# Kernel tuning notes

Hardware: AMD Instinct MI355X
Metric: run time of the kernel (lower is better)

The kernel has to match this reference:

```python
import jax, jax.numpy as jnp
import numpy as np
from jax import lax

WEIGHT_PREC = 8
ACT_PREC = 8
ACT_BOUND = 6.0  # fixed symmetric activation bound (quant_act.bounds)
EPS = 1e-6


def _ste_round(v):
    # AQT round-to-nearest with straight-through estimator
    return v + lax.stop_gradient(jnp.floor(v + 0.5) - v)


def setup_inputs() -> dict:
    key = jax.random.key(0)
    k1, k2 = jax.random.split(key)
    B, D, F = 131072, 512, 512
    x = jax.random.normal(k1, (B, D), dtype=jnp.float32)
    # lecun_normal-style kernel init
    kernel = jax.random.normal(k2, (D, F), dtype=jnp.float32) * (1.0 / np.sqrt(D))
    bias = jnp.zeros((F,), dtype=jnp.float32)
    padding_mask = jnp.ones((B, 1), dtype=bool)
    return {"x": x, "kernel": kernel, "bias": bias, "padding_mask": padding_mask}


def reference(x, kernel, bias, padding_mask):
    # padding_mask only affects bounds statistics collection; with fixed act
    # bounds and train=False it does not enter the math.
    wmax = float(2 ** (WEIGHT_PREC - 1) - 1)  # 127
    amax = float(2 ** (ACT_PREC - 1) - 1)     # 127

    # per-channel weight quantization: axis=(0,), scale shape (1, features)
    w_bound = jnp.maximum(jnp.max(jnp.abs(kernel), axis=0, keepdims=True), EPS)
    w_scale = wmax / w_bound                   # (1, F)
    w_q = jnp.clip(_ste_round(kernel * w_scale), -wmax, wmax)

    # per-tensor symmetric activation quantization with fixed bound
    a_scale = amax / ACT_BOUND                 # scalar
    x_q = jnp.clip(_ste_round(x * a_scale), -amax, amax)

    # integer-valued dot_general, then dequantize by the combined scale
    y = jnp.einsum('bd,df->bf', x_q, w_q)      # [B, F]
    y = y / (a_scale * w_scale)                # broadcast (1, F)
    return y + bias[jnp.newaxis, :]
```

## Files before the change

### kernel.cpp

```cpp
#include <hip/hip_runtime.h>
#include <stdint.h>

typedef int   int32x4   __attribute__((ext_vector_type(4)));
typedef int   int32x16  __attribute__((ext_vector_type(16)));
typedef float floatx4   __attribute__((ext_vector_type(4)));

#define B_ROWS 131072
#define DK 512
#define FN 512
#define A_SCALE_F ((float)(127.0 / 6.0))

#define GBLK 256
#define GT   1024
#define BMS  32
#define GTILES (B_ROWS / BMS / GBLK)

__global__ void wq_quant_kernel(const float* __restrict__ kern,
                                int8_t* __restrict__ wq,
                                float* __restrict__ invcs) {
  __shared__ float smax[256];
  __shared__ float sscale[4];
  const int c = threadIdx.x & 3;
  const int g = threadIdx.x >> 2;
  const int col = blockIdx.x * 4 + c;

  float m = 0.f;
#pragma unroll
  for (int i = 0; i < 8; ++i) {
    m = fmaxf(m, fabsf(kern[(size_t)(g * 8 + i) * FN + col]));
  }
  smax[threadIdx.x] = m;
  __syncthreads();
  if (threadIdx.x < 4) {
    float mm = smax[threadIdx.x];
#pragma unroll 8
    for (int g2 = 1; g2 < 64; ++g2) mm = fmaxf(mm, smax[g2 * 4 + threadIdx.x]);
    const float wb = fmaxf(mm, 1e-6f);
    const float ws = 127.f / wb;
    sscale[threadIdx.x] = ws;
    invcs[blockIdx.x * 4 + threadIdx.x] =
        (float)(1.0 / ((double)A_SCALE_F * (double)ws));
  }
  __syncthreads();
  const float ws = sscale[c];
  uint32_t* wq32 = (uint32_t*)(wq + (size_t)col * DK);
#pragma unroll
  for (int d = 0; d < 2; ++d) {
    uint32_t p = 0;
#pragma unroll
    for (int j = 0; j < 4; ++j) {
      float v = kern[(size_t)(g * 8 + d * 4 + j) * FN + col] * ws;
      v = floorf(v + 0.5f);
      v = fminf(fmaxf(v, -127.f), 127.f);
      p |= ((uint32_t)((int)v & 255)) << (8 * j);
    }
    wq32[g * 2 + d] = p;
  }
}

__global__ __launch_bounds__(GT, 4)
void aqt_gemm_fused(const float* __restrict__ x,
                    const int8_t* __restrict__ wq,
                    const float* __restrict__ invcs,
                    const float* __restrict__ bias,
                    float* __restrict__ out) {
  __shared__ __align__(16) uint8_t xq[2][BMS * DK];

  const int tid  = threadIdx.x;
  const int lane = tid & 63;
  const int wv   = tid >> 6;
  const int l31  = lane & 31;
  const int l5   = lane >> 5;

  const int c4 = tid & 127;
  const int r0 = tid >> 7;

  const int col = wv * 32 + l31;
  int32x4 Bf[16];
#pragma unroll
  for (int ks = 0; ks < 16; ++ks)
    Bf[ks] = *(const int32x4*)(wq + (size_t)col * DK + ks * 32 + l5 * 16);
  const float inv = invcs[col];
  const float bv  = bias[col];

  const size_t row0 = (size_t)blockIdx.x * (GTILES * BMS);

  {
    const float* xg = x + row0 * DK;
    floatx4 v[4];
#pragma unroll
    for (int i = 0; i < 4; ++i)
      v[i] = *(const floatx4*)(xg + (size_t)(i * 8 + r0) * DK + c4 * 4);
#pragma unroll
    for (int i = 0; i < 4; ++i) {
      const int r = i * 8 + r0;
      uint32_t p = 0;
#pragma unroll
      for (int j = 0; j < 4; ++j) {
        float q = floorf(v[i][j] * A_SCALE_F + 0.5f);
        q = fminf(fmaxf(q, -127.f), 127.f);
        p |= ((uint32_t)((int)q & 255)) << (8 * j);
      }
      *(uint32_t*)(&xq[0][r * DK + ((c4 * 4) ^ ((r & 31) << 4))]) = p;
    }
  }
  asm volatile("s_waitcnt lgkmcnt(0)" ::: "memory");
  __builtin_amdgcn_s_barrier();

  for (int t = 0; t < GTILES; ++t) {
    const uint8_t* bufC = &xq[t & 1][0];
    uint8_t* bufN = &xq[(t & 1) ^ 1][0];
    const size_t rowT = row0 + (size_t)t * BMS;
    const bool pf = (t + 1 < GTILES);

    floatx4 v[4];
    if (pf) {
      const float* xg = x + (rowT + BMS) * DK;
#pragma unroll
      for (int i = 0; i < 4; ++i)
        v[i] = *(const floatx4*)(xg + (size_t)(i * 8 + r0) * DK + c4 * 4);
    }

    int32x16 acc = (int32x16)(0);
    const uint8_t* aRow = bufC + l31 * DK;
    const int aswz = l31 << 4;
#pragma unroll
    for (int ks = 0; ks < 16; ++ks) {
      int32x4 a = *(const int32x4*)(aRow + ((ks * 32 + l5 * 16) ^ aswz));
      acc = __builtin_amdgcn_mfma_i32_32x32x32_i8(a, Bf[ks], acc, 0, 0, 0);
    }

    if (pf) {
#pragma unroll
      for (int i = 0; i < 4; ++i) {
        const int r = i * 8 + r0;
        uint32_t p = 0;
#pragma unroll
        for (int j = 0; j < 4; ++j) {
          float q = floorf(v[i][j] * A_SCALE_F + 0.5f);
          q = fminf(fmaxf(q, -127.f), 127.f);
          p |= ((uint32_t)((int)q & 255)) << (8 * j);
        }
        *(uint32_t*)(&bufN[r * DK + ((c4 * 4) ^ ((r & 31) << 4))]) = p;
      }
    }

#pragma unroll
    for (int r = 0; r < 16; ++r) {
      const int rowl = (r & 3) + 8 * (r >> 2) + 4 * l5;
      out[(rowT + rowl) * FN + col] = (float)acc[r] * inv + bv;
    }

    asm volatile("s_waitcnt lgkmcnt(0)" ::: "memory");
    __builtin_amdgcn_s_barrier();
  }
}

extern "C" void kernel_launch(void* const* d_in, const int* in_sizes, int n_in,
                              void* d_out, int out_size, void* d_ws, size_t ws_size,
                              hipStream_t stream) {
  const float* x    = (const float*)d_in[0];
  const float* kern = (const float*)d_in[1];
  const float* bias = (const float*)d_in[2];

  int8_t* wq    = (int8_t*)d_ws;
  float*  invcs = (float*)((char*)d_ws + (size_t)FN * DK);

  wq_quant_kernel<<<128, 256, 0, stream>>>(kern, wq, invcs);
  aqt_gemm_fused<<<GBLK, GT, 0, stream>>>(x, wq, invcs, bias, (float*)d_out);
}
```

Baseline: 131.9 us.

## Deepen global-load prefetch to two tiles ahead with unrolled ping-pong loop

```diff
diff --git a/kernel.cpp b/kernel.cpp
--- a/kernel.cpp
+++ b/kernel.cpp
@@ -58,6 +58,17 @@
   }
 }
 
+__device__ __forceinline__ uint32_t quant4(floatx4 v) {
+  uint32_t p = 0;
+#pragma unroll
+  for (int j = 0; j < 4; ++j) {
+    float q = floorf(v[j] * A_SCALE_F + 0.5f);
+    q = fminf(fmaxf(q, -127.f), 127.f);
+    p |= ((uint32_t)((int)q & 255)) << (8 * j);
+  }
+  return p;
+}
+
 __global__ __launch_bounds__(GT, 4)
 void aqt_gemm_fused(const float* __restrict__ x,
                     const int8_t* __restrict__ wq,
@@ -85,75 +96,68 @@
 
   const size_t row0 = (size_t)blockIdx.x * (GTILES * BMS);
 
-  {
-    const float* xg = x + row0 * DK;
-    floatx4 v[4];
-#pragma unroll
-    for (int i = 0; i < 4; ++i)
-      v[i] = *(const floatx4*)(xg + (size_t)(i * 8 + r0) * DK + c4 * 4);
-#pragma unroll
-    for (int i = 0; i < 4; ++i) {
-      const int r = i * 8 + r0;
-      uint32_t p = 0;
-#pragma unroll
-      for (int j = 0; j < 4; ++j) {
-        float q = floorf(v[i][j] * A_SCALE_F + 0.5f);
-        q = fminf(fmaxf(q, -127.f), 127.f);
-        p |= ((uint32_t)((int)q & 255)) << (8 * j);
-      }
-      *(uint32_t*)(&xq[0][r * DK + ((c4 * 4) ^ ((r & 31) << 4))]) = p;
-    }
+#define LOADV(vdst, rt)                                                       \
+  {                                                                           \
+    const float* xg_ = x + (size_t)(rt) * DK;                                 \
+    _Pragma("unroll")                                                         \
+    for (int i_ = 0; i_ < 4; ++i_)                                            \
+      vdst[i_] = *(const floatx4*)(xg_ + (size_t)(i_ * 8 + r0) * DK + c4 * 4);\
   }
+
+#define QWRITE(vsrc, bufp)                                                    \
+  {                                                                           \
+    _Pragma("unroll")                                                         \
+    for (int i_ = 0; i_ < 4; ++i_) {                                          \
+      const int r_ = i_ * 8 + r0;                                             \
+      *(uint32_t*)(&(bufp)[r_ * DK + ((c4 * 4) ^ ((r_ & 31) << 4))]) =        \
+          quant4(vsrc[i_]);                                                   \
+    }                                                                         \
+  }
+
+#define COMPUTE_STORE(bufp, rt)                                               \
+  {                                                                           \
+    int32x16 acc = (int32x16)(0);                                             \
+    const uint8_t* aRow_ = (bufp) + l31 * DK;                                 \
+    _Pragma("unroll")                                                         \
+    for (int ks_ = 0; ks_ < 16; ++ks_) {                                      \
+      int32x4 a_ = *(const int32x4*)(aRow_ + ((ks_ * 32 + l5 * 16) ^ (l31 << 4))); \
+      acc = __builtin_amdgcn_mfma_i32_32x32x32_i8(a_, Bf[ks_], acc, 0, 0, 0); \
+    }                                                                         \
+    _Pragma("unroll")                                                         \
+    for (int r_ = 0; r_ < 16; ++r_) {                                         \
+      const int rowl_ = (r_ & 3) + 8 * (r_ >> 2) + 4 * l5;                    \
+      out[((rt) + rowl_) * FN + col] = (float)acc[r_] * inv + bv;             \
+    }                                                                         \
+  }
+
+  floatx4 vA[4], vB[4];
+
+  LOADV(vA, row0);
+  QWRITE(vA, (&xq[0][0]));
+  LOADV(vB, row0 + BMS);
   asm volatile("s_waitcnt lgkmcnt(0)" ::: "memory");
   __builtin_amdgcn_s_barrier();
 
-  for (int t = 0; t < GTILES; ++t) {
-    const uint8_t* bufC = &xq[t & 1][0];
-    uint8_t* bufN = &xq[(t & 1) ^ 1][0];
+#pragma unroll 1
+  for (int t = 0; t < GTILES; t += 2) {
     const size_t rowT = row0 + (size_t)t * BMS;
-    const bool pf = (t + 1 < GTILES);
 
-    floatx4 v[4];
-    if (pf) {
-      const float* xg = x + (rowT + BMS) * DK;
-#pragma unroll
-      for (int i = 0; i < 4; ++i)
-        v[i] = *(const floatx4*)(xg + (size_t)(i * 8 + r0) * DK + c4 * 4);
-    }
+    if (t + 2 < GTILES) LOADV(vA, rowT + 2 * BMS);
+    COMPUTE_STORE((&xq[0][0]), rowT);
+    QWRITE(vB, (&xq[1][0]));
+    asm volatile("s_waitcnt lgkmcnt(0)" ::: "memory");
+    __builtin_amdgcn_s_barrier();
 
-    int32x16 acc = (int32x16)(0);
-    const uint8_t* aRow = bufC + l31 * DK;
-    const int aswz = l31 << 4;
-#pragma unroll
-    for (int ks = 0; ks < 16; ++ks) {
-      int32x4 a = *(const int32x4*)(aRow + ((ks * 32 + l5 * 16) ^ aswz));
-      acc = __builtin_amdgcn_mfma_i32_32x32x32_i8(a, Bf[ks], acc, 0, 0, 0);
-    }
-
-    if (pf) {
-#pragma unroll
-      for (int i = 0; i < 4; ++i) {
-        const int r = i * 8 + r0;
-        uint32_t p = 0;
-#pragma unroll
-        for (int j = 0; j < 4; ++j) {
-          float q = floorf(v[i][j] * A_SCALE_F + 0.5f);
-          q = fminf(fmaxf(q, -127.f), 127.f);
-          p |= ((uint32_t)((int)q & 255)) << (8 * j);
-        }
-        *(uint32_t*)(&bufN[r * DK + ((c4 * 4) ^ ((r & 31) << 4))]) = p;
-      }
-    }
-
-#pragma unroll
-    for (int r = 0; r < 16; ++r) {
-      const int rowl = (r & 3) + 8 * (r >> 2) + 4 * l5;
-      out[(rowT + rowl) * FN + col] = (float)acc[r] * inv + bv;
-    }
-
+    if (t + 3 < GTILES) LOADV(vB, rowT + 3 * BMS);
+    COMPUTE_STORE((&xq[1][0]), rowT + BMS);
+    if (t + 2 < GTILES) QWRITE(vA, (&xq[0][0]));
     asm volatile("s_waitcnt lgkmcnt(0)" ::: "memory");
     __builtin_amdgcn_s_barrier();
   }
+
+#undef LOADV
+#undef QWRITE
+#undef COMPUTE_STORE
 }
 
 extern "C" void kernel_launch(void* const* d_in, const int* in_sizes, int n_in,
```

Measured after the change: 188.4 us. 42.9% more time.
